# Performance work log

Measured on AMD Instinct MI355X. Metric: run time of the kernel, lower is better.

## Reference

```python
import jax, jax.numpy as jnp
import numpy as np
from jax.scipy.special import logsumexp

B, T, V, E, F, H, L = 64, 512, 30000, 256, 256, 256, 9
DROPOUT_RATE, DROPOUT_ROUND = 0.1, 4


def setup_inputs() -> dict:
    key = jax.random.key(0)
    ks = jax.random.split(key, 20)
    lengths = jax.random.randint(ks[0], (B,), T // 2, T + 1)
    tok = jax.random.randint(ks[1], (B, T), 1, V)
    input_ids = jnp.where(jnp.arange(T)[None, :] < lengths[:, None], tok, 0).astype(jnp.int32)
    labels = jax.random.randint(ks[2], (B, T), 0, L).astype(jnp.int32)
    W_emb = (jax.random.normal(ks[3], (V, E)) * 0.1).at[0].set(0.0)  # padding_idx=0 row zeroed
    w0 = jax.random.normal(ks[4], (F, F, 3)) * 0.05
    w1 = jax.random.normal(ks[5], (F, F, 3)) * 0.05
    w2 = jax.random.normal(ks[6], (F, F, 3)) * 0.05
    Wl = jax.random.normal(ks[7], (E, F)) * 0.05
    Wh = jax.random.normal(ks[8], (F, H)) * 0.05
    Wfc = jax.random.normal(ks[9], (H, L)) * 0.05
    crf_start = jax.random.normal(ks[10], (L,)) * 0.1
    crf_end = jax.random.normal(ks[11], (L,)) * 0.1
    crf_trans = jax.random.normal(ks[12], (L, L)) * 0.1
    z = jnp.zeros
    return dict(input_ids=input_ids, labels=labels, W_emb=W_emb,
                w0=w0, b0=z((F,)), w1=w1, b1=z((F,)), w2=w2, b2=z((F,)),
                Wl=Wl, bl=z((F,)), Wh=Wh, bh=z((H,)), Wfc=Wfc, bfc=z((L,)),
                crf_start=crf_start, crf_end=crf_end, crf_trans=crf_trans)


def _conv1d(x, w, b, dil):
    # x: [B, C, T]; w: [O, I, K]; 'same' padding given kernel 3 / dilation
    pad = 1 + dil - 1  # kernel_size//2 + dilation - 1
    y = jax.lax.conv_general_dilated(x, w, window_strides=(1,), padding=[(pad, pad)],
                                     rhs_dilation=(dil,), dimension_numbers=('NCH', 'OIH', 'NCH'))
    return y + b[None, :, None]


def reference(input_ids, labels, W_emb, w0, b0, w1, b1, w2, b2,
              Wl, bl, Wh, bh, Wfc, bfc, crf_start, crf_end, crf_trans):
    mask = input_ids > 0  # [B,T] bool, mask[:,0] all True by construction

    # --- encoder: embedding + IDCNN ---
    emb = W_emb[input_ids]                       # [B,T,E]
    x = (emb @ Wl + bl).transpose(0, 2, 1)       # [B,F,T]

    def block(h):  # faithful to add_module name collision: conv0 -> relu -> conv1 -> conv2
        h = _conv1d(h, w0, b0, 1)
        h = jax.nn.relu(h)
        h = _conv1d(h, w1, b1, 1)
        h = _conv1d(h, w2, b2, 2)
        return h

    x = block(x)
    x = jax.nn.relu(x)
    x = block(x)
    x = block(x)
    x = block(x)

    out = x.transpose(0, 2, 1) @ Wh + bh         # [B,T,H]

    # --- multisample dropout + fc (deterministic masks via fixed keys) ---
    keep = 1.0 - DROPOUT_RATE
    logits = jnp.zeros((B, T, L), dtype=out.dtype)
    for r in range(DROPOUT_ROUND):
        m = jax.random.bernoulli(jax.random.fold_in(jax.random.key(42), r), keep, out.shape)
        logits = logits + ((out * m / keep) @ Wfc + bfc)
    logits = logits / DROPOUT_ROUND              # [B,T,L] emissions

    # --- CRF negative log-likelihood (reduction='sum') ---
    fmask = mask.astype(logits.dtype)

    # numerator: score of gold path
    emit_sc = jnp.take_along_axis(logits, labels[..., None], axis=-1)[..., 0]  # [B,T]
    trans_sc = crf_trans[labels[:, :-1], labels[:, 1:]]                        # [B,T-1]
    numer = crf_start[labels[:, 0]] + emit_sc[:, 0]
    numer = numer + jnp.sum((trans_sc + emit_sc[:, 1:]) * fmask[:, 1:], axis=1)
    seq_ends = jnp.sum(mask, axis=1).astype(jnp.int32) - 1
    last_tags = labels[jnp.arange(B), seq_ends]
    numer = numer + crf_end[last_tags]

    # denominator: forward algorithm (sequential scan over time)
    alpha0 = crf_start[None, :] + logits[:, 0]   # [B,L]

    def step(alpha, xs):
        em_t, m_t = xs                            # [B,L], [B]
        nxt = logsumexp(alpha[:, :, None] + crf_trans[None] + em_t[:, None, :], axis=1)
        alpha = jnp.where(m_t[:, None], nxt, alpha)
        return alpha, None

    alpha, _ = jax.lax.scan(step, alpha0, (logits[:, 1:].transpose(1, 0, 2), mask[:, 1:].T))
    denom = logsumexp(alpha + crf_end[None, :], axis=1)

    loss = jnp.sum(denom - numer)  # = -crf.llh(sum)
    return loss
```

## Files before the change

kernel.cpp:

```cpp
#include <hip/hip_runtime.h>
#include <stdint.h>

#define B_ 64
#define T_ 512
#define V_ 30000
#define E_ 256
#define F_ 256
#define H_ 256
#define L_ 9
#define TP_ 516
#define M_ (B_*T_)
#define HALF_ ((B_*T_*H_)/2)
#define NCHUNK_ 64

typedef float f32x4 __attribute__((ext_vector_type(4)));
typedef __bf16 bf16x8 __attribute__((ext_vector_type(8)));

typedef __attribute__((address_space(3))) unsigned int lds_uint;
typedef __attribute__((address_space(1))) const unsigned int glob_uint;

__device__ __forceinline__ unsigned short f2b(float f) {
  unsigned u = __float_as_uint(f);
  unsigned r = (u + 0x7FFFu + ((u >> 16) & 1u)) >> 16;
  return (unsigned short)r;
}
__device__ __forceinline__ unsigned pack2(float a, float b) {
  return (unsigned)f2b(a) | ((unsigned)f2b(b) << 16);
}

__device__ __forceinline__ void threefry2x32(unsigned k0, unsigned k1,
                                             unsigned x0, unsigned x1,
                                             unsigned &o0, unsigned &o1) {
  unsigned ks2 = k0 ^ k1 ^ 0x1BD11BDAu;
  x0 += k0; x1 += k1;
#define TFR(r) { x0 += x1; x1 = (x1 << r) | (x1 >> (32 - r)); x1 ^= x0; }
  TFR(13) TFR(15) TFR(26) TFR(6)   x0 += k1;  x1 += ks2 + 1u;
  TFR(17) TFR(29) TFR(16) TFR(24)  x0 += ks2; x1 += k0 + 2u;
  TFR(13) TFR(15) TFR(26) TFR(6)   x0 += k0;  x1 += k1 + 3u;
  TFR(17) TFR(29) TFR(16) TFR(24)  x0 += k1;  x1 += ks2 + 4u;
  TFR(13) TFR(15) TFR(26) TFR(6)   x0 += ks2; x1 += k0 + 5u;
#undef TFR
  o0 = x0; o1 = x1;
}
__device__ __forceinline__ int keepbit(unsigned bits) {
  float u = __uint_as_float((bits >> 9) | 0x3F800000u) - 1.0f;
  return u < 0.9f ? 1 : 0;
}

__global__ __launch_bounds__(256) void zero_pads(unsigned short* xb0, unsigned short* xb1) {
  int idx = blockIdx.x * 256 + threadIdx.x;
  int b = idx >> 10, rr = (idx >> 8) & 3, f = idx & 255;
  int row = (rr < 2) ? rr : 512 + rr;
  int o = (b * TP_ + row) * 256 + f;
  xb0[o] = 0; xb1[o] = 0;
}

__global__ __launch_bounds__(256) void prep_convw(const float* __restrict__ w,
                                                  unsigned short* __restrict__ BT) {
  int idx = blockIdx.x * 256 + threadIdx.x;
  if (idx < F_ * 768) {
    int o = idx / 768;
    int rem = idx - o * 768;
    int kk = rem >> 8;
    int i = rem & 255;
    BT[idx] = f2b(w[(o * 256 + i) * 3 + kk]);
  }
}

__global__ __launch_bounds__(256) void prep_mat(const float* __restrict__ Wm,
                                                unsigned short* __restrict__ BT) {
  int idx = blockIdx.x * 256 + threadIdx.x;
  int f = idx >> 8, e = idx & 255;
  BT[idx] = f2b(Wm[e * 256 + f]);
}

__global__ void foldkeys(unsigned* fk) {
  if (threadIdx.x == 0 && blockIdx.x == 0) {
    for (int r = 0; r < 4; ++r) {
      unsigned o0, o1;
      threefry2x32(0u, 42u, 0u, (unsigned)r, o0, o1);
      fk[2 * r] = o0; fk[2 * r + 1] = o1;
    }
  }
}

template<int DIL, bool RELU>
__global__ __launch_bounds__(256, 2)
void conv3_gemm(const unsigned short* __restrict__ xin,
                const unsigned short* __restrict__ BT,
                const float* __restrict__ bias,
                unsigned short* __restrict__ xout) {
  __shared__ unsigned short Al[132 * 32];
  __shared__ unsigned short Bl[3 * 128 * 32];
  const int tid = threadIdx.x;
  const int tm = blockIdx.x, tn = blockIdx.y;
  const int lane = tid & 63, wid = tid >> 6;
  const int wm = wid >> 1, wn = wid & 1;
  const int fr = lane & 15, fq = lane >> 4;

  const int r0 = tm * 128;
  const int bb0 = r0 >> 9, t0 = r0 & 511;
  const int pb = bb0 * TP_ + t0;

  int aoff[2];
#pragma unroll
  for (int s = 0; s < 2; ++s) {
    int c = s * 256 + tid;
    aoff[s] = (pb + (c >> 2)) * 256 + (c & 3) * 8;
  }
  const int hoff = (pb + 128 + (tid >> 2)) * 256 + (tid & 3) * 8;
  int boff[6];
#pragma unroll
  for (int s = 0; s < 6; ++s) {
    int c = s * 256 + tid;
    boff[s] = (tn * 128 + ((c >> 2) & 127)) * 768 + (c >> 9) * 256 + (c & 3) * 8;
  }
  unsigned short* abase[2];
  unsigned short* bbase[6];
#pragma unroll
  for (int s = 0; s < 2; ++s) abase[s] = Al + (s * 256 + wid * 64) * 8;
#pragma unroll
  for (int s = 0; s < 6; ++s) bbase[s] = Bl + (s * 256 + wid * 64) * 8;

  f32x4 acc[4][4] = {};

  for (int kin = 0; kin < 256; kin += 32) {
#pragma unroll
    for (int s = 0; s < 2; ++s)
      __builtin_amdgcn_global_load_lds((glob_uint*)(xin + aoff[s] + kin),
                                       (lds_uint*)(abase[s]), 16, 0, 0);
#pragma unroll
    for (int s = 0; s < 6; ++s)
      __builtin_amdgcn_global_load_lds((glob_uint*)(BT + boff[s] + kin),
                                       (lds_uint*)(bbase[s]), 16, 0, 0);
    if (tid < 16) {
      uint4 v = *(const uint4*)(xin + hoff + kin);
      *(uint4*)(&Al[(128 + (tid >> 2)) * 32 + (tid & 3) * 8]) = v;
    }
    __syncthreads();
#pragma unroll
    for (int tp = 0; tp < 3; ++tp) {
      const int sh = (tp - 1) * DIL;
      bf16x8 af[4], bfv[4];
#pragma unroll
      for (int m = 0; m < 4; ++m)
        af[m] = *(const bf16x8*)(&Al[(wm * 64 + m * 16 + fr + 2 + sh) * 32 + fq * 8]);
#pragma unroll
      for (int n = 0; n < 4; ++n)
        bfv[n] = *(const bf16x8*)(&Bl[(tp * 128 + wn * 64 + n * 16 + fr) * 32 + fq * 8]);
#pragma unroll
      for (int m = 0; m < 4; ++m)
#pragma unroll
        for (int n = 0; n < 4; ++n)
          acc[m][n] = __builtin_amdgcn_mfma_f32_16x16x32_bf16(af[m], bfv[n], acc[m][n], 0, 0, 0);
    }
    __syncthreads();
  }

#pragma unroll
  for (int n = 0; n < 4; ++n) {
    const int col = tn * 128 + wn * 64 + n * 16 + fr;
    const float bs = bias[col];
#pragma unroll
    for (int m = 0; m < 4; ++m) {
      const int row0 = tm * 128 + wm * 64 + m * 16 + fq * 4;
#pragma unroll
      for (int rg = 0; rg < 4; ++rg) {
        const int row = row0 + rg;
        float x = acc[m][n][rg] + bs;
        if (RELU) x = fmaxf(x, 0.f);
        int bb = row >> 9, t = row & 511;
        xout[(bb * TP_ + t + 2) * 256 + col] = f2b(x);
      }
    }
  }
}

__global__ __launch_bounds__(256, 2)
void head_lin(const unsigned short* __restrict__ xin,
              const unsigned short* __restrict__ BTh,
              const float* __restrict__ bh,
              float* __restrict__ outf) {
  __shared__ unsigned short Al[128 * 32];
  __shared__ unsigned short Bl[128 * 32];
  const int tid = threadIdx.x;
  const int tm = blockIdx.x, tn = blockIdx.y;
  const int lane = tid & 63, wid = tid >> 6;
  const int wm = wid >> 1, wn = wid & 1;
  const int fr = lane & 15, fq = lane >> 4;

  int aoff[2], boff[2];
#pragma unroll
  for (int s = 0; s < 2; ++s) {
    int c = s * 256 + tid;
    int rr = c >> 2, q = c & 3;
    int r = tm * 128 + rr;
    aoff[s] = ((r >> 9) * TP_ + (r & 511) + 2) * 256 + q * 8;
    boff[s] = (tn * 128 + rr) * 256 + q * 8;
  }
  unsigned short *ab[2], *bb[2];
#pragma unroll
  for (int s = 0; s < 2; ++s) {
    ab[s] = Al + (s * 256 + wid * 64) * 8;
    bb[s] = Bl + (s * 256 + wid * 64) * 8;
  }

  f32x4 acc[4][4] = {};

  for (int kin = 0; kin < 256; kin += 32) {
#pragma unroll
    for (int s = 0; s < 2; ++s) {
      __builtin_amdgcn_global_load_lds((glob_uint*)(xin + aoff[s] + kin),
                                       (lds_uint*)(ab[s]), 16, 0, 0);
      __builtin_amdgcn_global_load_lds((glob_uint*)(BTh + boff[s] + kin),
                                       (lds_uint*)(bb[s]), 16, 0, 0);
    }
    __syncthreads();
    bf16x8 af[4], bfv[4];
#pragma unroll
    for (int m = 0; m < 4; ++m)
      af[m] = *(const bf16x8*)(&Al[(wm * 64 + m * 16 + fr) * 32 + fq * 8]);
#pragma unroll
    for (int n = 0; n < 4; ++n)
      bfv[n] = *(const bf16x8*)(&Bl[(wn * 64 + n * 16 + fr) * 32 + fq * 8]);
#pragma unroll
    for (int m = 0; m < 4; ++m)
#pragma unroll
      for (int n = 0; n < 4; ++n)
        acc[m][n] = __builtin_amdgcn_mfma_f32_16x16x32_bf16(af[m], bfv[n], acc[m][n], 0, 0, 0);
    __syncthreads();
  }

#pragma unroll
  for (int n = 0; n < 4; ++n) {
    const int col = tn * 128 + wn * 64 + n * 16 + fr;
    const float bs = bh[col];
#pragma unroll
    for (int m = 0; m < 4; ++m) {
      const int row0 = tm * 128 + wm * 64 + m * 16 + fq * 4;
#pragma unroll
      for (int rg = 0; rg < 4; ++rg)
        outf[(size_t)(row0 + rg) * H_ + col] = acc[m][n][rg] + bs;
    }
  }
}

__global__ __launch_bounds__(256) void head_fused2(const float* __restrict__ outf,
                                                   const float* __restrict__ Wfc,
                                                   const float* __restrict__ bfc,
                                                   const unsigned* __restrict__ fkg,
                                                   float* __restrict__ logits) {
  __shared__ float sW[H_ * L_];
  __shared__ float sB[L_];
  int tid = threadIdx.x;
  for (int i = tid; i < H_ * L_; i += 256) sW[i] = Wfc[i];
  if (tid < L_) sB[tid] = bfc[tid];
  __syncthreads();
  int wid = tid >> 6, lane = tid & 63;
  int r = blockIdx.x * 4 + wid;
  int r2 = r + M_ / 2;
  unsigned fk0[4], fk1[4];
#pragma unroll
  for (int rr = 0; rr < 4; ++rr) { fk0[rr] = fkg[2 * rr]; fk1[rr] = fkg[2 * rr + 1]; }
  float a0[L_] = {}, a1[L_] = {};
  const float sc = 1.0f / 3.6f;
#pragma unroll
  for (int e = 0; e < 4; ++e) {
    int h = lane + 64 * e;
    float x0v = outf[(size_t)r * 256 + h];
    float x1v = outf[(size_t)r2 * 256 + h];
    unsigned j = (unsigned)(r * 256 + h);
    int c0 = 0, c1 = 0;
#pragma unroll
    for (int rr = 0; rr < 4; ++rr) {
      unsigned o0, o1;
      threefry2x32(fk0[rr], fk1[rr], j, j + (unsigned)HALF_, o0, o1);
      c0 += keepbit(o0); c1 += keepbit(o1);
    }
    float x0 = x0v * (float)c0 * sc;
    float x1 = x1v * (float)c1 * sc;
#pragma unroll
    for (int c = 0; c < L_; ++c) {
      float w = sW[h * L_ + c];
      a0[c] = fmaf(x0, w, a0[c]);
      a1[c] = fmaf(x1, w, a1[c]);
    }
  }
#pragma unroll
  for (int c = 0; c < L_; ++c) {
#pragma unroll
    for (int off = 32; off; off >>= 1) {
      a0[c] += __shfl_down(a0[c], off);
      a1[c] += __shfl_down(a1[c], off);
    }
  }
  if (lane == 0) {
#pragma unroll
    for (int c = 0; c < L_; ++c) {
      logits[(size_t)r * L_ + c]  = a0[c] + sB[c];
      logits[(size_t)r2 * L_ + c] = a1[c] + sB[c];
    }
  }
}

__global__ __launch_bounds__(256) void crf_numer(const int* __restrict__ ids,
                                                 const int* __restrict__ labels,
                                                 const float* __restrict__ logits,
                                                 const float* __restrict__ cstart,
                                                 const float* __restrict__ cend,
                                                 const float* __restrict__ ctrans,
                                                 float* __restrict__ numer) {
  int b = blockIdx.x, tid = threadIdx.x;
  __shared__ float rs[256];
  __shared__ int rc[256];
  float p = 0.f; int cnt = 0;
  for (int t = tid; t < T_; t += 256) {
    int lab = labels[b * T_ + t];
    float em = logits[(b * T_ + t) * L_ + lab];
    int mk = ids[b * T_ + t] > 0;
    cnt += mk;
    if (t == 0) {
      p += cstart[lab] + em;
    } else if (mk) {
      int lp = labels[b * T_ + t - 1];
      p += ctrans[lp * L_ + lab] + em;
    }
  }
  rs[tid] = p; rc[tid] = cnt;
  __syncthreads();
  for (int s = 128; s > 0; s >>= 1) {
    if (tid < s) { rs[tid] += rs[tid + s]; rc[tid] += rc[tid + s]; }
    __syncthreads();
  }
  if (tid == 0) {
    int se = rc[0] - 1;
    int lt = labels[b * T_ + se];
    numer[b] = rs[0] + cend[lt];
  }
}

__global__ __launch_bounds__(128) void crf_chunk(const int* __restrict__ ids,
                                                 const float* __restrict__ logits,
                                                 const float* __restrict__ ctrans,
                                                 float* __restrict__ mats) {
  int blk = blockIdx.x;
  int b = blk >> 6, c = blk & 63;
  int e = threadIdx.x;
  int i = e / 9, j = e - 9 * i;
  __shared__ float cur[81];
  __shared__ float em[8 * 9];
  __shared__ int mk[8];
  int t0 = 8 * c;
  if (e < 72) em[e] = logits[((size_t)b * T_ + t0) * L_ + e];
  if (e < 8) mk[e] = (t0 + e >= 1) ? (ids[b * T_ + t0 + e] > 0) : 0;
  bool act = e < 81;
  float tcol[9];
  if (act) {
#pragma unroll
    for (int k = 0; k < 9; ++k) tcol[k] = ctrans[k * 9 + j];
    cur[e] = (i == j) ? 0.f : -1e30f;
  }
  __syncthreads();
  for (int s = 0; s < 8; ++s) {
    if (mk[s]) {
      float nv = 0.f;
      if (act) {
        float vv[9], mx = -3e38f;
#pragma unroll
        for (int k = 0; k < 9; ++k) { vv[k] = cur[i * 9 + k] + tcol[k]; mx = fmaxf(mx, vv[k]); }
        float ss = 0.f;
#pragma unroll
        for (int k = 0; k < 9; ++k) ss += __expf(vv[k] - mx);
        nv = mx + __logf(ss) + em[s * 9 + j];
      }
      __syncthreads();
      if (act) cur[e] = nv;
      __syncthreads();
    }
  }
  if (act) mats[(size_t)blk * 81 + e] = cur[e];
}

__global__ __launch_bounds__(256) void crf_combine(const float* __restrict__ mats,
                                                   const float* __restrict__ logits,
                                                   const float* __restrict__ cstart,
                                                   const float* __restrict__ cend,
                                                   const float* __restrict__ numer,
                                                   float* __restrict__ parts) {
  int b = blockIdx.x;
  __shared__ float bufA[64 * 81];
  __shared__ float bufB[32 * 81];
  __shared__ float alphaT[L_];
  int tid = threadIdx.x;
  for (int x = tid; x < 64 * 81; x += 256) bufA[x] = mats[(size_t)b * 64 * 81 + x];
  __syncthreads();
  float* src = bufA;
  float* dst = bufB;
  for (int n = 32; n >= 1; n >>= 1) {
    for (int x = tid; x < n * 81; x += 256) {
      int p = x / 81, e = x - 81 * p;
      int i = e / 9, j = e - 9 * i;
      const float* Lm = src + 162 * p;
      const float* Rm = Lm + 81;
      float vv[9], mx = -3e38f;
#pragma unroll
      for (int k = 0; k < 9; ++k) { vv[k] = Lm[i * 9 + k] + Rm[k * 9 + j]; mx = fmaxf(mx, vv[k]); }
      float ss = 0.f;
#pragma unroll
      for (int k = 0; k < 9; ++k) ss += __expf(vv[k] - mx);
      dst[x] = mx + __logf(ss);
    }
    __syncthreads();
    float* tmp = src; src = dst; dst = tmp;
  }
  const float* M = src;
  if (tid < L_) {
    int j = tid;
    float vv[9], mx = -3e38f;
#pragma unroll
    for (int i = 0; i < 9; ++i) {
      float a0 = cstart[i] + logits[(size_t)b * T_ * L_ + i];
      vv[i] = a0 + M[i * 9 + j];
      mx = fmaxf(mx, vv[i]);
    }
    float ss = 0.f;
#pragma unroll
    for (int i = 0; i < 9; ++i) ss += __expf(vv[i] - mx);
    alphaT[j] = mx + __logf(ss) + cend[j];
  }
  __syncthreads();
  if (tid == 0) {
    float mx = -3e38f;
#pragma unroll
    for (int j = 0; j < 9; ++j) mx = fmaxf(mx, alphaT[j]);
    float ss = 0.f;
#pragma unroll
    for (int j = 0; j < 9; ++j) ss += __expf(alphaT[j] - mx);
    parts[b] = mx + __logf(ss) - numer[b];
  }
}

__global__ void final_reduce(const float* __restrict__ parts, float* __restrict__ out) {
  int tid = threadIdx.x;
  float v = parts[tid];
#pragma unroll
  for (int off = 32; off; off >>= 1) v += __shfl_down(v, off);
  if (tid == 0) out[0] = v;
}

__global__ __launch_bounds__(256, 2)
void embed_gemm(const int* __restrict__ ids,
                const float* __restrict__ Wemb,
                const unsigned short* __restrict__ BT,
                const float* __restrict__ bias,
                unsigned short* __restrict__ xout) {
  __shared__ unsigned short Al[128 * 40];
  __shared__ unsigned short Bl[128 * 40];
  const int tid = threadIdx.x;
  const int tm = blockIdx.x, tn = blockIdx.y;
  const int lane = tid & 63, wid = tid >> 6;
  const int wm = wid >> 1, wn = wid & 1;
  const int fr = lane & 15, fq = lane >> 4;

  int asrc[2], boff[2], loff[2];
#pragma unroll
  for (int it = 0; it < 2; ++it) {
    int e = it * 256 + tid;
    int row = e >> 2, kq = e & 3;
    int r = tm * 128 + row;
    asrc[it] = ids[r] * E_ + kq * 8;
    boff[it] = (tn * 128 + row) * E_ + kq * 8;
    loff[it] = row * 40 + kq * 8;
  }

  f32x4 acc[4][4] = {};

  for (int k0 = 0; k0 < E_; k0 += 32) {
#pragma unroll
    for (int it = 0; it < 2; ++it) {
      const float* s = Wemb + asrc[it] + k0;
      float4 v0 = *(const float4*)s;
      float4 v1 = *(const float4*)(s + 4);
      uint4 va;
      va.x = pack2(v0.x, v0.y); va.y = pack2(v0.z, v0.w);
      va.z = pack2(v1.x, v1.y); va.w = pack2(v1.z, v1.w);
      uint4 vb = *(const uint4*)(BT + boff[it] + k0);
      *(uint4*)(&Al[loff[it]]) = va;
      *(uint4*)(&Bl[loff[it]]) = vb;
    }
    __syncthreads();
    bf16x8 af[4], bfv[4];
#pragma unroll
    for (int m = 0; m < 4; ++m)
      af[m] = *(const bf16x8*)(&Al[(wm * 64 + m * 16 + fr) * 40 + fq * 8]);
#pragma unroll
    for (int n = 0; n < 4; ++n)
      bfv[n] = *(const bf16x8*)(&Bl[(wn * 64 + n * 16 + fr) * 40 + fq * 8]);
#pragma unroll
    for (int m = 0; m < 4; ++m)
#pragma unroll
      for (int n = 0; n < 4; ++n)
        acc[m][n] = __builtin_amdgcn_mfma_f32_16x16x32_bf16(af[m], bfv[n], acc[m][n], 0, 0, 0);
    __syncthreads();
  }

#pragma unroll
  for (int n = 0; n < 4; ++n) {
    const int col = tn * 128 + wn * 64 + n * 16 + fr;
    const float bs = bias[col];
#pragma unroll
    for (int m = 0; m < 4; ++m) {
      const int row0 = tm * 128 + wm * 64 + m * 16 + fq * 4;
#pragma unroll
      for (int rg = 0; rg < 4; ++rg) {
        const int row = row0 + rg;
        float x = acc[m][n][rg] + bs;
        int bb = row >> 9, t = row & 511;
        xout[(bb * TP_ + t + 2) * 256 + col] = f2b(x);
      }
    }
  }
}

extern "C" void kernel_launch(void* const* d_in, const int* in_sizes, int n_in,
                              void* d_out, int out_size, void* d_ws, size_t ws_size,
                              hipStream_t stream) {
  const int*   ids    = (const int*)d_in[0];
  const int*   labels = (const int*)d_in[1];
  const float* Wemb   = (const float*)d_in[2];
  const float* w0     = (const float*)d_in[3];
  const float* b0     = (const float*)d_in[4];
  const float* w1     = (const float*)d_in[5];
  const float* b1     = (const float*)d_in[6];
  const float* w2     = (const float*)d_in[7];
  const float* b2     = (const float*)d_in[8];
  const float* Wl     = (const float*)d_in[9];
  const float* bl     = (const float*)d_in[10];
  const float* Wh     = (const float*)d_in[11];
  const float* bh     = (const float*)d_in[12];
  const float* Wfc    = (const float*)d_in[13];
  const float* bfc    = (const float*)d_in[14];
  const float* cstart = (const float*)d_in[15];
  const float* cend   = (const float*)d_in[16];
  const float* ctrans = (const float*)d_in[17];

  char* ws = (char*)d_ws;
  size_t off = 0;
  auto alloc = [&](size_t bytes) -> void* {
    void* p = ws + off;
    off += (bytes + 255) & ~(size_t)255;
    return p;
  };
  unsigned short* xb0 = (unsigned short*)alloc((size_t)B_ * TP_ * F_ * 2);
  unsigned short* xb1 = (unsigned short*)alloc((size_t)B_ * TP_ * F_ * 2);
  unsigned short* BTl = (unsigned short*)alloc((size_t)E_ * F_ * 2);
  unsigned short* BT0 = (unsigned short*)alloc((size_t)F_ * 768 * 2);
  unsigned short* BT1 = (unsigned short*)alloc((size_t)F_ * 768 * 2);
  unsigned short* BT2 = (unsigned short*)alloc((size_t)F_ * 768 * 2);
  unsigned short* BTh = (unsigned short*)alloc((size_t)F_ * H_ * 2);
  float* outf   = (float*)alloc((size_t)M_ * H_ * 4);
  float* logits = (float*)alloc((size_t)M_ * L_ * 4);
  unsigned* fk  = (unsigned*)alloc(64);
  float* numer  = (float*)alloc(B_ * 4);
  float* parts  = (float*)alloc(B_ * 4);
  float* mats   = (float*)alloc((size_t)B_ * NCHUNK_ * 81 * 4);
  if (ws_size < off) return;

  zero_pads<<<256, 256, 0, stream>>>(xb0, xb1);
  prep_convw<<<768, 256, 0, stream>>>(w0, BT0);
  prep_convw<<<768, 256, 0, stream>>>(w1, BT1);
  prep_convw<<<768, 256, 0, stream>>>(w2, BT2);
  prep_mat<<<256, 256, 0, stream>>>(Wl, BTl);
  prep_mat<<<256, 256, 0, stream>>>(Wh, BTh);
  foldkeys<<<1, 64, 0, stream>>>(fk);

  dim3 grid(M_ / 128, F_ / 128);
  embed_gemm<<<grid, 256, 0, stream>>>(ids, Wemb, BTl, bl, xb0);

  conv3_gemm<1, true ><<<grid, 256, 0, stream>>>(xb0, BT0, b0, xb1);
  conv3_gemm<1, false><<<grid, 256, 0, stream>>>(xb1, BT1, b1, xb0);
  conv3_gemm<2, true ><<<grid, 256, 0, stream>>>(xb0, BT2, b2, xb1);
  conv3_gemm<1, true ><<<grid, 256, 0, stream>>>(xb1, BT0, b0, xb0);
  conv3_gemm<1, false><<<grid, 256, 0, stream>>>(xb0, BT1, b1, xb1);
  conv3_gemm<2, false><<<grid, 256, 0, stream>>>(xb1, BT2, b2, xb0);
  conv3_gemm<1, true ><<<grid, 256, 0, stream>>>(xb0, BT0, b0, xb1);
  conv3_gemm<1, false><<<grid, 256, 0, stream>>>(xb1, BT1, b1, xb0);
  conv3_gemm<2, false><<<grid, 256, 0, stream>>>(xb0, BT2, b2, xb1);
  conv3_gemm<1, true ><<<grid, 256, 0, stream>>>(xb1, BT0, b0, xb0);
  conv3_gemm<1, false><<<grid, 256, 0, stream>>>(xb0, BT1, b1, xb1);
  conv3_gemm<2, false><<<grid, 256, 0, stream>>>(xb1, BT2, b2, xb0);

  head_lin<<<grid, 256, 0, stream>>>(xb0, BTh, bh, outf);
  head_fused2<<<M_ / 8, 256, 0, stream>>>(outf, Wfc, bfc, fk, logits);

  crf_numer<<<B_, 256, 0, stream>>>(ids, labels, logits, cstart, cend, ctrans, numer);
  crf_chunk<<<B_ * NCHUNK_, 128, 0, stream>>>(ids, logits, ctrans, mats);
  crf_combine<<<B_, 256, 0, stream>>>(mats, logits, cstart, cend, numer, parts);
  final_reduce<<<1, 64, 0, stream>>>(parts, (float*)d_out);
}
```

Baseline: 331.9 us.

## Double-buffer conv GEMM LDS and precompute dropout keep-counts in separate kernel

The conv3 GEMM now uses two LDS buffers and issues the next k-slice's global-to-LDS loads before computing on the current one, so memory latency overlaps with MFMA work. The halo row load also moves to the async global_load_lds path. Dropout keep-counts are generated by a standalone threefry kernel into a byte buffer, written once per element. The head kernel then reads those bytes with vectorised loads and reduces across 16 lanes instead of 64. This adds an 8 MB mask buffer and doubles LDS use per conv block, which may reduce occupancy.

```diff
diff --git a/kernel.cpp b/kernel.cpp
--- a/kernel.cpp
+++ b/kernel.cpp
@@ -12,6 +12,8 @@
 #define M_ (B_*T_)
 #define HALF_ ((B_*T_*H_)/2)
 #define NCHUNK_ 64
+#define AELEM_ (132*32)
+#define BELEM_ (3*128*32)
 
 typedef float f32x4 __attribute__((ext_vector_type(4)));
 typedef __bf16 bf16x8 __attribute__((ext_vector_type(8)));
@@ -42,10 +44,6 @@
 #undef TFR
   o0 = x0; o1 = x1;
 }
-__device__ __forceinline__ int keepbit(unsigned bits) {
-  float u = __uint_as_float((bits >> 9) | 0x3F800000u) - 1.0f;
-  return u < 0.9f ? 1 : 0;
-}
 
 __global__ __launch_bounds__(256) void zero_pads(unsigned short* xb0, unsigned short* xb1) {
   int idx = blockIdx.x * 256 + threadIdx.x;
@@ -84,14 +82,38 @@
   }
 }
 
+__global__ __launch_bounds__(256) void dropout_mask(const unsigned* __restrict__ fkg,
+                                                    unsigned char* __restrict__ cnt) {
+  unsigned fk0[4], fk1[4];
+#pragma unroll
+  for (int r = 0; r < 4; ++r) { fk0[r] = fkg[2 * r]; fk1[r] = fkg[2 * r + 1]; }
+  const unsigned j0 = (blockIdx.x * 256 + threadIdx.x) * 4;
+  unsigned c0 = 0, c1 = 0;
+#pragma unroll
+  for (int e = 0; e < 4; ++e) {
+    unsigned a = 0, b = 0;
+#pragma unroll
+    for (int r = 0; r < 4; ++r) {
+      unsigned o0, o1;
+      threefry2x32(fk0[r], fk1[r], j0 + e, j0 + e + (unsigned)HALF_, o0, o1);
+      a += (o0 < 0xE6666600u) ? 1u : 0u;
+      b += (o1 < 0xE6666600u) ? 1u : 0u;
+    }
+    c0 |= a << (8 * e);
+    c1 |= b << (8 * e);
+  }
+  *(unsigned*)(cnt + j0) = c0;
+  *(unsigned*)(cnt + HALF_ + j0) = c1;
+}
+
 template<int DIL, bool RELU>
 __global__ __launch_bounds__(256, 2)
 void conv3_gemm(const unsigned short* __restrict__ xin,
                 const unsigned short* __restrict__ BT,
                 const float* __restrict__ bias,
                 unsigned short* __restrict__ xout) {
-  __shared__ unsigned short Al[132 * 32];
-  __shared__ unsigned short Bl[3 * 128 * 32];
+  __shared__ unsigned short Al[2 * AELEM_];
+  __shared__ unsigned short Bl[2 * BELEM_];
   const int tid = threadIdx.x;
   const int tm = blockIdx.x, tn = blockIdx.y;
   const int lane = tid & 63, wid = tid >> 6;
@@ -115,39 +137,47 @@
     int c = s * 256 + tid;
     boff[s] = (tn * 128 + ((c >> 2) & 127)) * 768 + (c >> 9) * 256 + (c & 3) * 8;
   }
-  unsigned short* abase[2];
-  unsigned short* bbase[6];
-#pragma unroll
-  for (int s = 0; s < 2; ++s) abase[s] = Al + (s * 256 + wid * 64) * 8;
-#pragma unroll
-  for (int s = 0; s < 6; ++s) bbase[s] = Bl + (s * 256 + wid * 64) * 8;
-
-  f32x4 acc[4][4] = {};
-
-  for (int kin = 0; kin < 256; kin += 32) {
+  const int aco[2] = {(0 * 256 + wid * 64) * 8, (1 * 256 + wid * 64) * 8};
+  int bco[6];
+#pragma unroll
+  for (int s = 0; s < 6; ++s) bco[s] = (s * 256 + wid * 64) * 8;
+
+  auto stage = [&](int p, int kin) {
+    unsigned short* Ab = Al + p * AELEM_;
+    unsigned short* Bb = Bl + p * BELEM_;
 #pragma unroll
     for (int s = 0; s < 2; ++s)
       __builtin_amdgcn_global_load_lds((glob_uint*)(xin + aoff[s] + kin),
-                                       (lds_uint*)(abase[s]), 16, 0, 0);
+                                       (lds_uint*)(Ab + aco[s]), 16, 0, 0);
 #pragma unroll
     for (int s = 0; s < 6; ++s)
       __builtin_amdgcn_global_load_lds((glob_uint*)(BT + boff[s] + kin),
-                                       (lds_uint*)(bbase[s]), 16, 0, 0);
-    if (tid < 16) {
-      uint4 v = *(const uint4*)(xin + hoff + kin);
-      *(uint4*)(&Al[(128 + (tid >> 2)) * 32 + (tid & 3) * 8]) = v;
-    }
-    __syncthreads();
+                                       (lds_uint*)(Bb + bco[s]), 16, 0, 0);
+    if (tid < 16)
+      __builtin_amdgcn_global_load_lds((glob_uint*)(xin + hoff + kin),
+                                       (lds_uint*)(Ab + 128 * 32), 16, 0, 0);
+  };
+
+  f32x4 acc[4][4] = {};
+
+  stage(0, 0);
+  __syncthreads();
+
+  for (int ks = 0; ks < 8; ++ks) {
+    const int cur = ks & 1;
+    if (ks < 7) stage(cur ^ 1, (ks + 1) * 32);
+    const unsigned short* Ab = Al + cur * AELEM_;
+    const unsigned short* Bb = Bl + cur * BELEM_;
 #pragma unroll
     for (int tp = 0; tp < 3; ++tp) {
       const int sh = (tp - 1) * DIL;
       bf16x8 af[4], bfv[4];
 #pragma unroll
       for (int m = 0; m < 4; ++m)
-        af[m] = *(const bf16x8*)(&Al[(wm * 64 + m * 16 + fr + 2 + sh) * 32 + fq * 8]);
+        af[m] = *(const bf16x8*)(&Ab[(wm * 64 + m * 16 + fr + 2 + sh) * 32 + fq * 8]);
 #pragma unroll
       for (int n = 0; n < 4; ++n)
-        bfv[n] = *(const bf16x8*)(&Bl[(tp * 128 + wn * 64 + n * 16 + fr) * 32 + fq * 8]);
+        bfv[n] = *(const bf16x8*)(&Bb[(tp * 128 + wn * 64 + n * 16 + fr) * 32 + fq * 8]);
 #pragma unroll
       for (int m = 0; m < 4; ++m)
 #pragma unroll
@@ -245,61 +275,45 @@
   }
 }
 
-__global__ __launch_bounds__(256) void head_fused2(const float* __restrict__ outf,
-                                                   const float* __restrict__ Wfc,
-                                                   const float* __restrict__ bfc,
-                                                   const unsigned* __restrict__ fkg,
-                                                   float* __restrict__ logits) {
+__global__ __launch_bounds__(256) void head_apply(const float* __restrict__ outf,
+                                                  const unsigned char* __restrict__ cnt,
+                                                  const float* __restrict__ Wfc,
+                                                  const float* __restrict__ bfc,
+                                                  float* __restrict__ logits) {
   __shared__ float sW[H_ * L_];
   __shared__ float sB[L_];
   int tid = threadIdx.x;
   for (int i = tid; i < H_ * L_; i += 256) sW[i] = Wfc[i];
   if (tid < L_) sB[tid] = bfc[tid];
   __syncthreads();
-  int wid = tid >> 6, lane = tid & 63;
-  int r = blockIdx.x * 4 + wid;
-  int r2 = r + M_ / 2;
-  unsigned fk0[4], fk1[4];
-#pragma unroll
-  for (int rr = 0; rr < 4; ++rr) { fk0[rr] = fkg[2 * rr]; fk1[rr] = fkg[2 * rr + 1]; }
-  float a0[L_] = {}, a1[L_] = {};
+  const int lane = tid & 63, wid = tid >> 6;
+  const int fr = lane & 15, g16 = lane >> 4;
+  const int row = blockIdx.x * 16 + wid * 4 + g16;
+  const float* orow = outf + (size_t)row * 256 + fr * 16;
+  const unsigned char* crow = cnt + (size_t)row * 256 + fr * 16;
+  uint4 cb = *(const uint4*)crow;
   const float sc = 1.0f / 3.6f;
-#pragma unroll
-  for (int e = 0; e < 4; ++e) {
-    int h = lane + 64 * e;
-    float x0v = outf[(size_t)r * 256 + h];
-    float x1v = outf[(size_t)r2 * 256 + h];
-    unsigned j = (unsigned)(r * 256 + h);
-    int c0 = 0, c1 = 0;
-#pragma unroll
-    for (int rr = 0; rr < 4; ++rr) {
-      unsigned o0, o1;
-      threefry2x32(fk0[rr], fk1[rr], j, j + (unsigned)HALF_, o0, o1);
-      c0 += keepbit(o0); c1 += keepbit(o1);
-    }
-    float x0 = x0v * (float)c0 * sc;
-    float x1 = x1v * (float)c1 * sc;
-#pragma unroll
-    for (int c = 0; c < L_; ++c) {
-      float w = sW[h * L_ + c];
-      a0[c] = fmaf(x0, w, a0[c]);
-      a1[c] = fmaf(x1, w, a1[c]);
-    }
-  }
-#pragma unroll
-  for (int c = 0; c < L_; ++c) {
-#pragma unroll
-    for (int off = 32; off; off >>= 1) {
-      a0[c] += __shfl_down(a0[c], off);
-      a1[c] += __shfl_down(a1[c], off);
-    }
-  }
-  if (lane == 0) {
-#pragma unroll
-    for (int c = 0; c < L_; ++c) {
-      logits[(size_t)r * L_ + c]  = a0[c] + sB[c];
-      logits[(size_t)r2 * L_ + c] = a1[c] + sB[c];
-    }
+  float a[9] = {};
+#pragma unroll
+  for (int q = 0; q < 4; ++q) {
+    float4 v = *(const float4*)(orow + q * 4);
+    unsigned cw = ((const unsigned*)&cb)[q];
+    float xs[4] = {v.x, v.y, v.z, v.w};
+#pragma unroll
+    for (int k = 0; k < 4; ++k) {
+      const int h = fr * 16 + q * 4 + k;
+      const float x = xs[k] * (float)((cw >> (8 * k)) & 255u) * sc;
+#pragma unroll
+      for (int c = 0; c < 9; ++c) a[c] = fmaf(x, sW[h * 9 + c], a[c]);
+    }
+  }
+#pragma unroll
+  for (int c = 0; c < 9; ++c)
+#pragma unroll
+    for (int o = 1; o < 16; o <<= 1) a[c] += __shfl_xor(a[c], o);
+  if (fr == 0) {
+#pragma unroll
+    for (int c = 0; c < 9; ++c) logits[(size_t)row * 9 + c] = a[c] + sB[c];
   }
 }
 
@@ -559,6 +573,7 @@
   unsigned short* BT2 = (unsigned short*)alloc((size_t)F_ * 768 * 2);
   unsigned short* BTh = (unsigned short*)alloc((size_t)F_ * H_ * 2);
   float* outf   = (float*)alloc((size_t)M_ * H_ * 4);
+  unsigned char* cntb = (unsigned char*)alloc((size_t)M_ * H_);
   float* logits = (float*)alloc((size_t)M_ * L_ * 4);
   unsigned* fk  = (unsigned*)alloc(64);
   float* numer  = (float*)alloc(B_ * 4);
@@ -573,6 +588,7 @@
   prep_mat<<<256, 256, 0, stream>>>(Wl, BTl);
   prep_mat<<<256, 256, 0, stream>>>(Wh, BTh);
   foldkeys<<<1, 64, 0, stream>>>(fk);
+  dropout_mask<<<HALF_ / 1024, 256, 0, stream>>>(fk, cntb);
 
   dim3 grid(M_ / 128, F_ / 128);
   embed_gemm<<<grid, 256, 0, stream>>>(ids, Wemb, BTl, bl, xb0);
@@ -591,7 +607,7 @@
   conv3_gemm<2, false><<<grid, 256, 0, stream>>>(xb1, BT2, b2, xb0);
 
   head_lin<<<grid, 256, 0, stream>>>(xb0, BTh, bh, outf);
-  head_fused2<<<M_ / 8, 256, 0, stream>>>(outf, Wfc, bfc, fk, logits);
+  head_apply<<<M_ / 16, 256, 0, stream>>>(outf, cntb, Wfc, bfc, logits);
 
   crf_numer<<<B_, 256, 0, stream>>>(ids, labels, logits, cstart, cend, ctrans, numer);
   crf_chunk<<<B_ * NCHUNK_, 128, 0, stream>>>(ids, logits, ctrans, mats);
```

After: 341.8 us. 1.03x slower.
